# Performance work log

Measured on AMD Instinct MI355X. Metric: run time of the kernel, lower is better.

The kernel has to match this reference:

```python
import jax, jax.numpy as jnp
import numpy as np

INF = 1e5
EPS = 1e-8
B, NRES, NRIG = 1, 448, 512
C_S, C_Z, C_H, H, PQ, PV = 384, 128, 16, 12, 4, 8


def _quat_to_rot(q):
    q = q / jnp.linalg.norm(q, axis=-1, keepdims=True)
    w, x, y, z = q[..., 0], q[..., 1], q[..., 2], q[..., 3]
    return jnp.stack([
        jnp.stack([1 - 2 * (y * y + z * z), 2 * (x * y - w * z), 2 * (x * z + w * y)], -1),
        jnp.stack([2 * (x * y + w * z), 1 - 2 * (x * x + z * z), 2 * (y * z - w * x)], -1),
        jnp.stack([2 * (x * z - w * y), 2 * (y * z + w * x), 1 - 2 * (x * x + y * y)], -1),
    ], -2)


def setup_inputs() -> dict:
    key = jax.random.key(0)
    ks = jax.random.split(key, 16)
    lin = lambda k, i, o: (jax.random.normal(k, (i, o), jnp.float32) / np.sqrt(i))
    hc = H * C_H
    return dict(
        s=jax.random.normal(ks[0], (B, NRIG, C_S), jnp.float32),
        z=jax.random.normal(ks[1], (B, NRES, NRES, C_Z), jnp.float32),
        rot=_quat_to_rot(jax.random.normal(ks[2], (B, NRIG, 4), jnp.float32)),
        trans=jax.random.normal(ks[3], (B, NRIG, 3), jnp.float32) * 10.0,
        mask=jnp.ones((B, NRIG), jnp.float32),
        rigid_to_res_idx=jax.random.randint(ks[4], (B, NRIG), 0, NRES),
        w_q=lin(ks[5], C_S, hc), b_q=jnp.zeros((hc,), jnp.float32),
        w_kv=lin(ks[6], C_S, 2 * hc), b_kv=jnp.zeros((2 * hc,), jnp.float32),
        w_qp=lin(ks[7], C_S, H * PQ * 3), b_qp=jnp.zeros((H * PQ * 3,), jnp.float32),
        w_kvp=lin(ks[8], C_S, H * (PQ + PV) * 3), b_kvp=jnp.zeros((H * (PQ + PV) * 3,), jnp.float32),
        w_b=lin(ks[9], C_Z, H), b_b=jnp.zeros((H,), jnp.float32),
        w_dz=lin(ks[10], C_Z, C_Z // 4), b_dz=jnp.zeros((C_Z // 4,), jnp.float32),
        head_weights=jnp.full((H,), 0.5413, jnp.float32),  # softplus^-1(1)
        w_out=lin(ks[11], H * (C_Z // 4 + C_H + PV * 4), C_S),
        b_out=jnp.zeros((C_S,), jnp.float32),
    )


def _fwd(s, z, rot, trans, mask, rigid_to_res_idx,
         w_q, b_q, w_kv, b_kv, w_qp, b_qp, w_kvp, b_kvp,
         w_b, b_b, w_dz, b_dz, head_weights, w_out, b_out):
    Bd, nr, _ = s.shape
    nres = z.shape[-2]
    h = w_b.shape[-1]
    ch = w_q.shape[-1] // h
    pq = w_qp.shape[-1] // (3 * h)
    pkv = w_kvp.shape[-1] // (3 * h)
    pv = pkv - pq

    q = (s @ w_q + b_q).reshape(Bd, nr, h, ch)
    kv = (s @ w_kv + b_kv).reshape(Bd, nr, h, 2 * ch)
    k, v = kv[..., :ch], kv[..., ch:]

    def to_pts(flat):
        # flat: [B,nr,3*D] laid out as 3 coordinate chunks -> global-frame pts [B,nr,D,3]
        D = flat.shape[-1] // 3
        p = jnp.moveaxis(flat.reshape(Bd, nr, 3, D), -2, -1)
        return jnp.einsum('bnij,bndj->bndi', rot, p) + trans[:, :, None, :]

    q_pts = to_pts(s @ w_qp + b_qp).reshape(Bd, nr, h, pq, 3)
    kv_pts = to_pts(s @ w_kvp + b_kvp).reshape(Bd, nr, h, pkv, 3)
    k_pts, v_pts = kv_pts[..., :pq, :], kv_pts[..., pq:, :]

    # pair bias gathered rigid->res on both axes
    bi = jnp.arange(Bd)[:, None, None]
    b_pair = z @ w_b + b_b  # [B,Nres,Nres,H]
    b_bcast = b_pair[bi, rigid_to_res_idx[:, :, None], rigid_to_res_idx[:, None, :]]  # [B,nr,nr,H]

    a = jnp.einsum('bihc,bjhc->bhij', q, k) * np.sqrt(1.0 / (3 * ch))
    a = a + np.sqrt(1.0 / 3) * jnp.moveaxis(b_bcast, -1, -3)

    # squared-distance point attention
    diff = q_pts[:, :, None] - k_pts[:, None]  # [B,nr,nr,h,pq,3]
    sq = jnp.sum(diff * diff, -1)              # [B,nr,nr,h,pq]
    hw = jax.nn.softplus(head_weights) * np.sqrt(1.0 / (3 * (pq * 9.0 / 2)))
    pt_att = -0.5 * jnp.sum(sq * hw[:, None], -1)  # [B,nr,nr,h]
    a = a + jnp.moveaxis(pt_att, -1, -3)

    sq_mask = INF * (mask[:, :, None] * mask[:, None, :] - 1.0)
    a = jax.nn.softmax(a + sq_mask[:, None], axis=-1)  # [B,h,nr,nr]

    o = jnp.einsum('bhij,bjhc->bihc', a, v).reshape(Bd, nr, h * ch)

    o_pt_g = jnp.einsum('bhij,bjhpx->bihpx', a, v_pts)  # [B,nr,h,pv,3]
    o_pt = jnp.einsum('bnji,bnhpj->bnhpi', rot, o_pt_g - trans[:, :, None, None, :])  # invert_apply
    o_pt_norm = jnp.sqrt(jnp.sum(o_pt * o_pt, -1) + EPS).reshape(Bd, nr, h * pv)
    o_pt = o_pt.reshape(Bd, nr, h * pv, 3)

    pair_z = z @ w_dz + b_dz  # [B,Nres,Nres,cz4]
    pz_rig = pair_z[jnp.arange(Bd)[:, None], rigid_to_res_idx]  # [B,nr,Nres,cz4]
    # faithful to the torch scatter_add_: the index varies over the QUERY rigid i
    # (constant over keys j), so row i's full softmax mass lands in column res(i).
    onehot = jax.nn.one_hot(rigid_to_res_idx, nres, dtype=a.dtype)  # [B,nr,Nres]
    a_agg = a.sum(-1)[..., None] * onehot[:, None]  # [B,h,nr,Nres]
    o_pair = jnp.einsum('bhin,bind->bihd', a_agg, pz_rig).reshape(Bd, nr, -1)

    feats = jnp.concatenate([o, o_pt[..., 0], o_pt[..., 1], o_pt[..., 2], o_pt_norm, o_pair], -1)
    return feats @ w_out + b_out


def reference(s, z, rot, trans, mask, rigid_to_res_idx, w_q, b_q, w_kv, b_kv, w_qp, b_qp, w_kvp, b_kvp, w_b, b_b, w_dz, b_dz, head_weights, w_out, b_out):
    return _fwd(s, z, rot, trans, mask, rigid_to_res_idx, w_q, b_q, w_kv, b_kv, w_qp, b_qp, w_kvp, b_kvp, w_b, b_b, w_dz, b_dz, head_weights, w_out, b_out)
```

## Files before the change

### kernel.cpp

```cpp
#include <hip/hip_runtime.h>
#include <hip/hip_bf16.h>
#include <math.h>

constexpr int NRIG = 512;
constexpr int NRES = 448;
constexpr int CS   = 384;
constexpr int CZ   = 128;
constexpr int CH   = 16;
constexpr int NH   = 12;
constexpr int PQ   = 4;
constexpr int PV   = 8;
constexpr int HC   = NH * CH;
constexpr float INF_ = 100000.0f;

constexpr size_t OFF_Q   = 0;
constexpr size_t OFF_K   = OFF_Q   + (size_t)NH*NRIG*16;
constexpr size_t OFF_QP  = OFF_K   + (size_t)NH*NRIG*16;
constexpr size_t OFF_KP  = OFF_QP  + (size_t)NH*NRIG*12;
constexpr size_t OFF_VT  = OFF_KP  + (size_t)NH*NRIG*12;
constexpr size_t OFF_PZ  = OFF_VT  + (size_t)NH*40*NRIG;
constexpr size_t OFF_O   = OFF_PZ  + (size_t)NRIG*32;
constexpr size_t OFF_OPT = OFF_O   + (size_t)NRIG*HC;
constexpr size_t OFF_RS  = OFF_OPT + (size_t)NRIG*NH*PV*3;
constexpr size_t OFF_B   = OFF_RS  + (size_t)NRIG*NH;
constexpr size_t OFF_RAW = OFF_B;

__global__ __launch_bounds__(256) void proj_gemm_kernel(
    const float* __restrict__ s,
    const float* __restrict__ wq,  const float* __restrict__ bq,
    const float* __restrict__ wkv, const float* __restrict__ bkv,
    const float* __restrict__ wqp, const float* __restrict__ bqp,
    const float* __restrict__ wkvp,const float* __restrict__ bkvp,
    float* __restrict__ ws)
{
    constexpr int BM=64, BN=32, BK=32, LDA=68;
    __shared__ float sA[BK][LDA];
    __shared__ float sB[BK][BN];
    const int m0 = blockIdx.x * BM;
    const int c0 = blockIdx.y * BN;
    const int t  = threadIdx.x;
    const int tx = t & 15, ty = t >> 4;

    float acc[4][2] = {};

    for (int kt = 0; kt < CS/BK; ++kt) {
        const int k0 = kt*BK;
        #pragma unroll
        for (int r = 0; r < 2; ++r) {
            int qd = r*256 + t;
            int m = qd >> 3, kq = (qd & 7) << 2;
            float4 f = *(const float4*)(s + (size_t)(m0+m)*CS + k0 + kq);
            sA[kq+0][m] = f.x; sA[kq+1][m] = f.y;
            sA[kq+2][m] = f.z; sA[kq+3][m] = f.w;
        }
        {
            int kk = t >> 3, c4 = (t & 7) << 2;
            int c = c0 + c4;
            const float* wp; int ld, co;
            if (c < 192)      { wp = wq;   ld = 192; co = c;     }
            else if (c < 576) { wp = wkv;  ld = 384; co = c-192; }
            else if (c < 720) { wp = wqp;  ld = 144; co = c-576; }
            else              { wp = wkvp; ld = 432; co = c-720; }
            float4 f = *(const float4*)(wp + (size_t)(k0+kk)*ld + co);
            *(float4*)&sB[kk][c4] = f;
        }
        __syncthreads();
        #pragma unroll
        for (int kk = 0; kk < BK; ++kk) {
            float4 a = *(const float4*)&sA[kk][ty*4];
            float2 b = *(const float2*)&sB[kk][tx*2];
            acc[0][0] += a.x*b.x; acc[0][1] += a.x*b.y;
            acc[1][0] += a.y*b.x; acc[1][1] += a.y*b.y;
            acc[2][0] += a.z*b.x; acc[2][1] += a.z*b.y;
            acc[3][0] += a.w*b.x; acc[3][1] += a.w*b.y;
        }
        __syncthreads();
    }

    float* qw  = ws + OFF_Q;  float* kw = ws + OFF_K;  float* vt = ws + OFF_VT;
    float* raw = ws + OFF_RAW;
    #pragma unroll
    for (int i = 0; i < 4; ++i)
        #pragma unroll
        for (int j = 0; j < 2; ++j) {
            int n = m0 + ty*4 + i;
            int c = c0 + tx*2 + j;
            if (c < 192) {
                int hh = c >> 4, cc = c & 15;
                qw[((size_t)hh*NRIG + n)*16 + cc] = acc[i][j] + bq[c];
            } else if (c < 576) {
                int e = c-192; float val = acc[i][j] + bkv[e];
                int hh = e >> 5, sub = e & 31;
                if (sub < CH) kw[((size_t)hh*NRIG + n)*16 + sub] = val;
                else          vt[((size_t)hh*40 + (sub-CH))*NRIG + n] = val;
            } else {
                int e = c-576;
                float bb_ = (c < 720) ? bqp[e] : bkvp[c-720];
                raw[(size_t)n*576 + e] = acc[i][j] + bb_;
            }
        }
}

__global__ __launch_bounds__(256) void rotate_kernel(
    const float* __restrict__ rot, const float* __restrict__ trans,
    float* __restrict__ ws)
{
    const int gid = blockIdx.x*256 + threadIdx.x;
    const int n = gid / 192, d = gid % 192;
    const float* raw = ws + OFF_RAW + (size_t)n*576;
    float px, py, pzz;
    if (d < 48) { px = raw[d];      py = raw[48+d];       pzz = raw[96+d]; }
    else { int dd = d-48; px = raw[144+dd]; py = raw[288+dd]; pzz = raw[432+dd]; }
    const float* R = rot   + (size_t)n*9;
    const float* T = trans + (size_t)n*3;
    float gx = R[0]*px + R[1]*py + R[2]*pzz + T[0];
    float gy = R[3]*px + R[4]*py + R[5]*pzz + T[1];
    float gz = R[6]*px + R[7]*py + R[8]*pzz + T[2];
    if (d < 48) {
        int hh = d >> 2, pp = d & 3;
        float* dst = ws + OFF_QP + ((size_t)hh*NRIG + n)*12 + pp*3;
        dst[0]=gx; dst[1]=gy; dst[2]=gz;
    } else {
        int dd = d-48; int hh = dd/12, pp = dd%12;
        if (pp < PQ) {
            float* dst = ws + OFF_KP + ((size_t)hh*NRIG + n)*12 + pp*3;
            dst[0]=gx; dst[1]=gy; dst[2]=gz;
        } else {
            float* vt = ws + OFF_VT + ((size_t)hh*40 + 16 + (pp-PQ)*3)*NRIG + n;
            vt[0*NRIG]=gx; vt[1*NRIG]=gy; vt[2*NRIG]=gz;
        }
    }
}

__global__ __launch_bounds__(256) void bpair_kernel(
    const float* __restrict__ z, const int* __restrict__ ridx,
    const float* __restrict__ wb, const float* __restrict__ bb,
    const float* __restrict__ wdz, const float* __restrict__ bdz,
    float* __restrict__ ws)
{
    __shared__ float4 sWb[CZ*3];
    __shared__ float sZd[CZ];
    const int t = threadIdx.x;
    const int i = blockIdx.x;
    const int ri = ridx[i];
    for (int e = t; e < CZ*3; e += 256) sWb[e] = ((const float4*)wb)[e];
    if (t < CZ) sZd[t] = z[((size_t)ri*NRES + ri)*CZ + t];
    __syncthreads();

    const int j0  = t, j1 = t + 256;
    const int rj0 = ridx[j0], rj1 = ridx[j1];
    const float4* zr0 = (const float4*)(z + ((size_t)ri*NRES + rj0)*CZ);
    const float4* zr1 = (const float4*)(z + ((size_t)ri*NRES + rj1)*CZ);

    float a0[12], a1[12];
    #pragma unroll
    for (int hh=0; hh<12; ++hh) { a0[hh]=0.f; a1[hh]=0.f; }

    #pragma unroll 4
    for (int c4 = 0; c4 < 32; ++c4) {
        float4 z0 = zr0[c4], z1 = zr1[c4];
        #pragma unroll
        for (int e = 0; e < 4; ++e) {
            const int c = (c4<<2) + e;
            float wv[12];
            *(float4*)&wv[0] = sWb[c*3+0];
            *(float4*)&wv[4] = sWb[c*3+1];
            *(float4*)&wv[8] = sWb[c*3+2];
            const float zv0 = (&z0.x)[e];
            const float zv1 = (&z1.x)[e];
            #pragma unroll
            for (int hh=0; hh<12; ++hh) { a0[hh] += zv0*wv[hh]; a1[hh] += zv1*wv[hh]; }
        }
    }
    const float SC = 0.57735026918962584f;
    float* bbc = ws + OFF_B;
    #pragma unroll
    for (int hh = 0; hh < 12; ++hh) {
        float bias = bb[hh];
        bbc[((size_t)hh*NRIG + i)*NRIG + j0] = (a0[hh]+bias)*SC;
        bbc[((size_t)hh*NRIG + i)*NRIG + j1] = (a1[hh]+bias)*SC;
    }
    if (t < 32) {
        float acc = 0.f;
        for (int c = 0; c < CZ; ++c) acc += sZd[c] * wdz[(size_t)c*32 + t];
        (ws + OFF_PZ)[(size_t)i*32 + t] = acc + bdz[t];
    }
}

__global__ __launch_bounds__(256) void attn_kernel(
    const float* __restrict__ hw_in, const float* __restrict__ mask,
    float* __restrict__ ws)
{
    constexpr int TI = 4;
    const int h    = blockIdx.x;
    const int i0   = blockIdx.y * TI;
    const int t    = threadIdx.x;
    const int lane = t & 63, wid = t >> 6;

    __shared__ float sQ[TI][16];
    __shared__ float sQP[TI][12];
    __shared__ float sE[TI][512];
    __shared__ float redM[TI][4], redS[TI][4];
    __shared__ float sMi[TI];
    __shared__ float sP[TI][16][44];

    const float* qw  = ws + OFF_Q  + (size_t)h*NRIG*16;
    const float* kw  = ws + OFF_K  + (size_t)h*NRIG*16;
    const float* qpw = ws + OFF_QP + (size_t)h*NRIG*12;
    const float* kpw = ws + OFF_KP + (size_t)h*NRIG*12;
    const float* vt  = ws + OFF_VT + (size_t)h*40*NRIG;
    const float* bbc = ws + OFF_B  + (size_t)h*NRIG*NRIG;

    for (int e = t; e < TI*16; e += 256) sQ[e/16][e%16]  = qw[(size_t)(i0+e/16)*16 + (e%16)];
    for (int e = t; e < TI*12; e += 256) sQP[e/12][e%12] = qpw[(size_t)(i0+e/12)*12 + (e%12)];
    if (t < TI) sMi[t] = mask[i0+t];
    __syncthreads();

    const float hwv = -0.5f * log1pf(__expf(hw_in[h])) * 0.13608276348795434f;
    const float QKS = 0.14433756729740643f;

    float lg[2][TI];
    float lmax[TI] = {-1e30f,-1e30f,-1e30f,-1e30f};
    #pragma unroll
    for (int jj = 0; jj < 2; ++jj) {
        int j = t + jj*256;
        float kk[16], kpv[12];
        const float4* kr = (const float4*)(kw + (size_t)j*16);
        *(float4*)&kk[0]=kr[0]; *(float4*)&kk[4]=kr[1]; *(float4*)&kk[8]=kr[2]; *(float4*)&kk[12]=kr[3];
        const float4* kpr = (const float4*)(kpw + (size_t)j*12);
        *(float4*)&kpv[0]=kpr[0]; *(float4*)&kpv[4]=kpr[1]; *(float4*)&kpv[8]=kpr[2];
        float mj = mask[j];
        #pragma unroll
        for (int qq = 0; qq < TI; ++qq) {
            float dot = 0.f;
            #pragma unroll
            for (int c = 0; c < 16; ++c) dot += sQ[qq][c]*kk[c];
            float sq = 0.f;
            #pragma unroll
            for (int e = 0; e < 12; ++e) { float d = sQP[qq][e]-kpv[e]; sq += d*d; }
            float bv = bbc[(size_t)(i0+qq)*NRIG + j];
            float lgt = dot*QKS + bv + hwv*sq + INF_*(sMi[qq]*mj - 1.0f);
            lg[jj][qq] = lgt;
            lmax[qq] = fmaxf(lmax[qq], lgt);
        }
    }
    #pragma unroll
    for (int sft = 1; sft < 64; sft <<= 1)
        #pragma unroll
        for (int qq=0;qq<TI;++qq) lmax[qq] = fmaxf(lmax[qq], __shfl_xor(lmax[qq], sft));
    if (lane == 0) { for (int qq=0;qq<TI;++qq) redM[qq][wid] = lmax[qq]; }
    __syncthreads();
    float M[TI], psum[TI];
    #pragma unroll
    for (int qq=0;qq<TI;++qq) {
        M[qq] = fmaxf(fmaxf(redM[qq][0],redM[qq][1]),fmaxf(redM[qq][2],redM[qq][3]));
        psum[qq]=0.f;
    }
    #pragma unroll
    for (int jj = 0; jj < 2; ++jj) {
        int j = t + jj*256;
        #pragma unroll
        for (int qq=0;qq<TI;++qq) {
            float e = __expf(lg[jj][qq] - M[qq]);
            sE[qq][j] = e;
            psum[qq] += e;
        }
    }
    #pragma unroll
    for (int sft = 1; sft < 64; sft <<= 1)
        #pragma unroll
        for (int qq=0;qq<TI;++qq) psum[qq] += __shfl_xor(psum[qq], sft);
    if (lane == 0) { for (int qq=0;qq<TI;++qq) redS[qq][wid] = psum[qq]; }
    __syncthreads();

    {
        const int c0 = wid*10;
        float acc[10][TI];
        #pragma unroll
        for (int ci=0;ci<10;++ci)
            #pragma unroll
            for (int qq=0;qq<TI;++qq) acc[ci][qq]=0.f;

        #pragma unroll
        for (int m = 0; m < 8; ++m) {
            const int j = lane + 64*m;
            float ev[TI];
            #pragma unroll
            for (int qq=0;qq<TI;++qq) ev[qq] = sE[qq][j];
            #pragma unroll
            for (int ci = 0; ci < 10; ++ci) {
                float vv = vt[(size_t)(c0+ci)*NRIG + j];
                #pragma unroll
                for (int qq=0;qq<TI;++qq) acc[ci][qq] += ev[qq]*vv;
            }
        }
        #pragma unroll
        for (int ci=0;ci<10;++ci)
            #pragma unroll
            for (int qq=0;qq<TI;++qq) {
                acc[ci][qq] += __shfl_xor(acc[ci][qq], 1);
                acc[ci][qq] += __shfl_xor(acc[ci][qq], 2);
            }
        if ((lane & 3) == 0) {
            const int g = lane >> 2;
            #pragma unroll
            for (int qq=0;qq<TI;++qq)
                #pragma unroll
                for (int ci=0;ci<10;++ci)
                    sP[qq][g][c0+ci] = acc[ci][qq];
        }
    }
    __syncthreads();

    if (t < TI*41) {
        const int qq = t / 41, c = t % 41;
        const int n = i0 + qq;
        float S = redS[qq][0]+redS[qq][1]+redS[qq][2]+redS[qq][3];
        float Sinv = 1.0f / S;
        if (c == 40) {
            (ws + OFF_RS)[(size_t)n*NH + h] = S * Sinv;
        } else {
            float acc = 0.f;
            #pragma unroll
            for (int g = 0; g < 16; ++g) acc += sP[qq][g][c];
            acc *= Sinv;
            if (c < 16) (ws + OFF_O  )[((size_t)n*NH + h)*CH + c]      = acc;
            else        (ws + OFF_OPT)[((size_t)n*NH + h)*24 + (c-16)] = acc;
        }
    }
}

__global__ __launch_bounds__(192) void out_kernel(
    const float* __restrict__ rot, const float* __restrict__ trans,
    const float* __restrict__ w_out, const float* __restrict__ b_out,
    const float* __restrict__ ws, float* __restrict__ out)
{
    constexpr int TI = 4;
    __shared__ float sF[TI][960];
    const int i0 = blockIdx.y*TI;
    const int c0 = blockIdx.x*192;
    const int t  = threadIdx.x;
    const float* o_ws = ws + OFF_O;  const float* optg = ws + OFF_OPT;
    const float* rs   = ws + OFF_RS; const float* pz   = ws + OFF_PZ;

    for (int e = t; e < TI*HC; e += 192)
        sF[e/HC][e%HC] = o_ws[(size_t)(i0 + e/HC)*HC + (e%HC)];
    for (int e = t; e < TI*96; e += 192) {
        int qq = e/96, hp = e%96; int n = i0+qq;
        const float* g = optg + ((size_t)n*NH + hp/PV)*24 + (hp%PV)*3;
        float gx = g[0]-trans[n*3+0], gy = g[1]-trans[n*3+1], gz = g[2]-trans[n*3+2];
        const float* R = rot + (size_t)n*9;
        float lx = R[0]*gx + R[3]*gy + R[6]*gz;
        float ly = R[1]*gx + R[4]*gy + R[7]*gz;
        float lz = R[2]*gx + R[5]*gy + R[8]*gz;
        sF[qq][192+hp] = lx; sF[qq][288+hp] = ly; sF[qq][384+hp] = lz;
        sF[qq][480+hp] = sqrtf(lx*lx+ly*ly+lz*lz + 1e-8f);
    }
    for (int e = t; e < TI*384; e += 192) {
        int qq = e/384, hd = e%384; int n = i0+qq;
        sF[qq][576+hd] = rs[(size_t)n*NH + hd/32] * pz[(size_t)n*32 + (hd%32)];
    }
    __syncthreads();

    const int col = c0 + t;
    float b = b_out[col];
    float a0=b, a1=b, a2=b, a3=b;
    for (int f = 0; f < 960; ++f) {
        float wv = w_out[(size_t)f*CS + col];
        a0 += sF[0][f]*wv; a1 += sF[1][f]*wv; a2 += sF[2][f]*wv; a3 += sF[3][f]*wv;
    }
    out[(size_t)(i0+0)*CS + col] = a0;
    out[(size_t)(i0+1)*CS + col] = a1;
    out[(size_t)(i0+2)*CS + col] = a2;
    out[(size_t)(i0+3)*CS + col] = a3;
}

extern "C" void kernel_launch(void* const* d_in, const int* in_sizes, int n_in,
                              void* d_out, int out_size, void* d_ws, size_t ws_size,
                              hipStream_t stream)
{
    const float* s     = (const float*)d_in[0];
    const float* z     = (const float*)d_in[1];
    const float* rot   = (const float*)d_in[2];
    const float* trans = (const float*)d_in[3];
    const float* mask  = (const float*)d_in[4];
    const int*   ridx  = (const int*)  d_in[5];
    const float* wq    = (const float*)d_in[6];
    const float* bq    = (const float*)d_in[7];
    const float* wkv   = (const float*)d_in[8];
    const float* bkv   = (const float*)d_in[9];
    const float* wqp   = (const float*)d_in[10];
    const float* bqp   = (const float*)d_in[11];
    const float* wkvp  = (const float*)d_in[12];
    const float* bkvp  = (const float*)d_in[13];
    const float* wb    = (const float*)d_in[14];
    const float* bb    = (const float*)d_in[15];
    const float* wdz   = (const float*)d_in[16];
    const float* bdz   = (const float*)d_in[17];
    const float* hw    = (const float*)d_in[18];
    const float* wout  = (const float*)d_in[19];
    const float* bout  = (const float*)d_in[20];
    float* ws  = (float*)d_ws;
    float* out = (float*)d_out;

    hipLaunchKernelGGL(proj_gemm_kernel, dim3(NRIG/64, 1152/32), dim3(256), 0, stream,
        s, wq,bq, wkv,bkv, wqp,bqp, wkvp,bkvp, ws);
    hipLaunchKernelGGL(rotate_kernel, dim3(NRIG*192/256), dim3(256), 0, stream,
        rot, trans, ws);
    hipLaunchKernelGGL(bpair_kernel, dim3(NRIG), dim3(256), 0, stream,
        z, ridx, wb, bb, wdz, bdz, ws);
    hipLaunchKernelGGL(attn_kernel, dim3(NH, NRIG/4), dim3(256), 0, stream,
        hw, mask, ws);
    hipLaunchKernelGGL(out_kernel, dim3(2, NRIG/4), dim3(192), 0, stream,
        rot, trans, wout, bout, ws, out);
}
```

Before: 127.9 us.

## Split output projection into feature-materialize kernel and tiled shared-memory GEMM

The fused out_kernel built a 4-row feature tile in shared memory and had each thread stream a full column of w_out, so w_out was reread by every 4-row block. The new code writes the 960-wide feature rows to workspace in a separate kernel, then runs a 64x32 register-tiled GEMM that reuses w_out across 64 rows. This adds one kernel launch and a round trip of the feature matrix through global memory. It also reuses the OFF_B workspace region, which is assumed to be dead by this point.

```diff
diff --git a/kernel.cpp b/kernel.cpp
--- a/kernel.cpp
+++ b/kernel.cpp
@@ -24,6 +24,7 @@
 constexpr size_t OFF_RS  = OFF_OPT + (size_t)NRIG*NH*PV*3;
 constexpr size_t OFF_B   = OFF_RS  + (size_t)NRIG*NH;
 constexpr size_t OFF_RAW = OFF_B;
+constexpr size_t OFF_F   = OFF_B;
 
 __global__ __launch_bounds__(256) void proj_gemm_kernel(
     const float* __restrict__ s,
@@ -330,22 +331,22 @@
     }
 }
 
-__global__ __launch_bounds__(192) void out_kernel(
+__global__ __launch_bounds__(256) void feats_kernel(
     const float* __restrict__ rot, const float* __restrict__ trans,
-    const float* __restrict__ w_out, const float* __restrict__ b_out,
-    const float* __restrict__ ws, float* __restrict__ out)
+    float* __restrict__ ws)
 {
     constexpr int TI = 4;
-    __shared__ float sF[TI][960];
-    const int i0 = blockIdx.y*TI;
-    const int c0 = blockIdx.x*192;
+    const int i0 = blockIdx.x*TI;
     const int t  = threadIdx.x;
+    float* F = ws + OFF_F;
     const float* o_ws = ws + OFF_O;  const float* optg = ws + OFF_OPT;
     const float* rs   = ws + OFF_RS; const float* pz   = ws + OFF_PZ;
 
-    for (int e = t; e < TI*HC; e += 192)
-        sF[e/HC][e%HC] = o_ws[(size_t)(i0 + e/HC)*HC + (e%HC)];
-    for (int e = t; e < TI*96; e += 192) {
+    for (int e = t; e < TI*HC; e += 256) {
+        int qq = e/HC, c = e%HC;
+        F[(size_t)(i0+qq)*960 + c] = o_ws[(size_t)(i0+qq)*HC + c];
+    }
+    for (int e = t; e < TI*96; e += 256) {
         int qq = e/96, hp = e%96; int n = i0+qq;
         const float* g = optg + ((size_t)n*NH + hp/PV)*24 + (hp%PV)*3;
         float gx = g[0]-trans[n*3+0], gy = g[1]-trans[n*3+1], gz = g[2]-trans[n*3+2];
@@ -353,26 +354,67 @@
         float lx = R[0]*gx + R[3]*gy + R[6]*gz;
         float ly = R[1]*gx + R[4]*gy + R[7]*gz;
         float lz = R[2]*gx + R[5]*gy + R[8]*gz;
-        sF[qq][192+hp] = lx; sF[qq][288+hp] = ly; sF[qq][384+hp] = lz;
-        sF[qq][480+hp] = sqrtf(lx*lx+ly*ly+lz*lz + 1e-8f);
-    }
-    for (int e = t; e < TI*384; e += 192) {
+        float* Fr = F + (size_t)n*960;
+        Fr[192+hp] = lx; Fr[288+hp] = ly; Fr[384+hp] = lz;
+        Fr[480+hp] = sqrtf(lx*lx+ly*ly+lz*lz + 1e-8f);
+    }
+    for (int e = t; e < TI*384; e += 256) {
         int qq = e/384, hd = e%384; int n = i0+qq;
-        sF[qq][576+hd] = rs[(size_t)n*NH + hd/32] * pz[(size_t)n*32 + (hd%32)];
-    }
-    __syncthreads();
-
-    const int col = c0 + t;
-    float b = b_out[col];
-    float a0=b, a1=b, a2=b, a3=b;
-    for (int f = 0; f < 960; ++f) {
-        float wv = w_out[(size_t)f*CS + col];
-        a0 += sF[0][f]*wv; a1 += sF[1][f]*wv; a2 += sF[2][f]*wv; a3 += sF[3][f]*wv;
-    }
-    out[(size_t)(i0+0)*CS + col] = a0;
-    out[(size_t)(i0+1)*CS + col] = a1;
-    out[(size_t)(i0+2)*CS + col] = a2;
-    out[(size_t)(i0+3)*CS + col] = a3;
+        F[(size_t)n*960 + 576 + hd] = rs[(size_t)n*NH + hd/32] * pz[(size_t)n*32 + (hd%32)];
+    }
+}
+
+__global__ __launch_bounds__(256) void out_gemm_kernel(
+    const float* __restrict__ w_out, const float* __restrict__ b_out,
+    const float* __restrict__ ws, float* __restrict__ out)
+{
+    constexpr int BM=64, BN=32, BK=32, LDA=68;
+    __shared__ float sA[BK][LDA];
+    __shared__ float sB[BK][BN];
+    const float* F = ws + OFF_F;
+    const int m0 = blockIdx.x * BM;
+    const int c0 = blockIdx.y * BN;
+    const int t  = threadIdx.x;
+    const int tx = t & 15, ty = t >> 4;
+
+    float acc[4][2] = {};
+
+    for (int kt = 0; kt < 960/BK; ++kt) {
+        const int k0 = kt*BK;
+        #pragma unroll
+        for (int r = 0; r < 2; ++r) {
+            int qd = r*256 + t;
+            int m = qd >> 3, kq = (qd & 7) << 2;
+            float4 f = *(const float4*)(F + (size_t)(m0+m)*960 + k0 + kq);
+            sA[kq+0][m] = f.x; sA[kq+1][m] = f.y;
+            sA[kq+2][m] = f.z; sA[kq+3][m] = f.w;
+        }
+        {
+            int kk = t >> 3, c4 = (t & 7) << 2;
+            float4 f = *(const float4*)(w_out + (size_t)(k0+kk)*CS + c0 + c4);
+            *(float4*)&sB[kk][c4] = f;
+        }
+        __syncthreads();
+        #pragma unroll
+        for (int kk = 0; kk < BK; ++kk) {
+            float4 a = *(const float4*)&sA[kk][ty*4];
+            float2 b = *(const float2*)&sB[kk][tx*2];
+            acc[0][0] += a.x*b.x; acc[0][1] += a.x*b.y;
+            acc[1][0] += a.y*b.x; acc[1][1] += a.y*b.y;
+            acc[2][0] += a.z*b.x; acc[2][1] += a.z*b.y;
+            acc[3][0] += a.w*b.x; acc[3][1] += a.w*b.y;
+        }
+        __syncthreads();
+    }
+
+    #pragma unroll
+    for (int i = 0; i < 4; ++i)
+        #pragma unroll
+        for (int j = 0; j < 2; ++j) {
+            int n = m0 + ty*4 + i;
+            int c = c0 + tx*2 + j;
+            out[(size_t)n*CS + c] = acc[i][j] + b_out[c];
+        }
 }
 
 extern "C" void kernel_launch(void* const* d_in, const int* in_sizes, int n_in,
@@ -411,6 +453,8 @@
         z, ridx, wb, bb, wdz, bdz, ws);
     hipLaunchKernelGGL(attn_kernel, dim3(NH, NRIG/4), dim3(256), 0, stream,
         hw, mask, ws);
-    hipLaunchKernelGGL(out_kernel, dim3(2, NRIG/4), dim3(192), 0, stream,
-        rot, trans, wout, bout, ws, out);
-}
+    hipLaunchKernelGGL(feats_kernel, dim3(NRIG/4), dim3(256), 0, stream,
+        rot, trans, ws);
+    hipLaunchKernelGGL(out_gemm_kernel, dim3(NRIG/64, CS/32), dim3(256), 0, stream,
+        wout, bout, ws, out);
+}
```

Result: faster. 122.0 us (-4.6%).
